# Kernel tuning notes

Measured on AMD Instinct MI355X. Metric: run time of the kernel, lower is better.

Reference implementation:

```python
import jax, jax.numpy as jnp
import numpy as np
from jax import lax

B = 65536
IMG = 28
K = 3
OUT_HW = IMG - K + 1  # 26
FLAT = OUT_HW * OUT_HW  # 676
HID = 100
NCLS = 10


def setup_inputs() -> dict:
    key = jax.random.key(0)
    ks = jax.random.split(key, 6)
    x = jax.random.normal(ks[0], (B, IMG * IMG), dtype=jnp.float32)
    conv_w = jax.random.normal(ks[1], (K, K), dtype=jnp.float32)
    # Linear params, PyTorch layout: weight [out, in], bias [out]
    w1 = jax.random.normal(ks[2], (HID, FLAT), dtype=jnp.float32) * (1.0 / np.sqrt(FLAT))
    b1 = jax.random.normal(ks[3], (HID,), dtype=jnp.float32) * 0.01
    w2 = jax.random.normal(ks[4], (NCLS, HID), dtype=jnp.float32) * (1.0 / np.sqrt(HID))
    b2 = jax.random.normal(ks[5], (NCLS,), dtype=jnp.float32) * 0.01
    return {"x": x, "conv_w": conv_w, "w1": w1, "b1": b1, "w2": w2, "b2": b2}


def reference(x, conv_w, w1, b1, w2, b2):
    # x: [B, 784] -> [B, 1, 28, 28]
    img = x.reshape(-1, 1, IMG, IMG)
    # Cross-correlation (matches the slice*weight sum in Convolve), valid padding
    kern = conv_w[None, None, :, :]  # [O=1, I=1, 3, 3]
    conv = lax.conv_general_dilated(
        img, kern, window_strides=(1, 1), padding="VALID",
        dimension_numbers=("NCHW", "OIHW", "NCHW"),
    )  # [B, 1, 26, 26]
    feat = conv.reshape(conv.shape[0], FLAT)
    h1 = jax.nn.relu(feat @ w1.T + b1)
    return h1 @ w2.T + b2  # [B, 10]
```

## Files before the change

kernel.cpp:

```cpp
#include <hip/hip_runtime.h>

#define IMG 28
#define FLATK 784
#define OHW 26
#define FLAT 676
#define HID 100
#define NCLS 10
#define KP 800
#define BM 128

typedef __attribute__((ext_vector_type(8))) short bfrag;
typedef __attribute__((ext_vector_type(4))) float f32x4;
typedef __attribute__((ext_vector_type(4))) unsigned int u32x4;

__device__ __forceinline__ unsigned short f2bf(float f) {
    unsigned u = __float_as_uint(f);
    u = (u + 0x7fffu + ((u >> 16) & 1u)) >> 16;
    return (unsigned short)u;
}

__global__ void build_weights(const float* __restrict__ conv_w,
                              const float* __restrict__ w1,
                              const float* __restrict__ w2,
                              unsigned short* __restrict__ w1b,
                              unsigned short* __restrict__ w2b) {
    int idx = blockIdx.x * blockDim.x + threadIdx.x;
    if (idx < 128 * KP) {
        int n = idx / KP, k = idx - n * KP;
        float val = 0.f;
        if (n < HID && k < FLATK) {
            int qr = k / IMG, qc = k % IMG;
            #pragma unroll
            for (int i = 0; i < 3; ++i) {
                int r = qr - i;
                if (r < 0 || r >= OHW) continue;
                #pragma unroll
                for (int j = 0; j < 3; ++j) {
                    int c = qc - j;
                    if (c < 0 || c >= OHW) continue;
                    val += conv_w[i * 3 + j] * w1[n * FLAT + r * OHW + c];
                }
            }
        }
        w1b[idx] = f2bf(val);
    } else {
        int t = idx - 128 * KP;
        if (t < 16 * 128) {
            int n = t >> 7, k = t & 127;
            float v = (n < NCLS && k < HID) ? w2[n * HID + k] : 0.f;
            w2b[t] = f2bf(v);
        }
    }
}

#define LOADA(PH, S) do {                                                      \
    int k_ = (S) * 32 + (khi << 3);                                            \
    if (k_ >= FLATK) k_ -= FLATK;     \
    pre[PH][0] = *(const f32x4*)(xr0 + k_);                                    \
    pre[PH][1] = *(const f32x4*)(xr0 + k_ + 4);                                \
    pre[PH][2] = *(const f32x4*)(xr1 + k_);                                    \
    pre[PH][3] = *(const f32x4*)(xr1 + k_ + 4);                                \
} while (0)

#define COMP(PH, S) do {                                                       \
    union { u32x4 u; bfrag b; } a0_, a1_;                                      \
    asm("v_cvt_pk_bf16_f32 %0, %1, %2" : "=v"(a0_.u.x) : "v"(pre[PH][0].x), "v"(pre[PH][0].y)); \
    asm("v_cvt_pk_bf16_f32 %0, %1, %2" : "=v"(a0_.u.y) : "v"(pre[PH][0].z), "v"(pre[PH][0].w)); \
    asm("v_cvt_pk_bf16_f32 %0, %1, %2" : "=v"(a0_.u.z) : "v"(pre[PH][1].x), "v"(pre[PH][1].y)); \
    asm("v_cvt_pk_bf16_f32 %0, %1, %2" : "=v"(a0_.u.w) : "v"(pre[PH][1].z), "v"(pre[PH][1].w)); \
    asm("v_cvt_pk_bf16_f32 %0, %1, %2" : "=v"(a1_.u.x) : "v"(pre[PH][2].x), "v"(pre[PH][2].y)); \
    asm("v_cvt_pk_bf16_f32 %0, %1, %2" : "=v"(a1_.u.y) : "v"(pre[PH][2].z), "v"(pre[PH][2].w)); \
    asm("v_cvt_pk_bf16_f32 %0, %1, %2" : "=v"(a1_.u.z) : "v"(pre[PH][3].x), "v"(pre[PH][3].y)); \
    asm("v_cvt_pk_bf16_f32 %0, %1, %2" : "=v"(a1_.u.w) : "v"(pre[PH][3].z), "v"(pre[PH][3].w)); \
    _Pragma("unroll")                                                          \
    for (int nt = 0; nt < 8; ++nt) {                                           \
        const bfrag bw = *(const bfrag*)(w1b + (size_t)((nt << 4) + r15) * KP  \
                                         + (S) * 32 + (khi << 3));             \
        acc0[nt] = __builtin_amdgcn_mfma_f32_16x16x32_bf16(a0_.b, bw, acc0[nt], 0, 0, 0); \
        acc1[nt] = __builtin_amdgcn_mfma_f32_16x16x32_bf16(a1_.b, bw, acc1[nt], 0, 0, 0); \
    }                                                                          \
} while (0)

__global__ __launch_bounds__(256) void fused_fwd(
    const float* __restrict__ x,
    const unsigned short* __restrict__ w1b,
    const float* __restrict__ b1,
    const unsigned short* __restrict__ w2b,
    const float* __restrict__ b2,
    float* __restrict__ out)
{
    __shared__ unsigned short H1[BM][136];

    const int tid  = threadIdx.x;
    const int lane = tid & 63;
    const int wv   = tid >> 6;
    const int r15  = lane & 15;
    const int khi  = lane >> 4;
    const int row0 = blockIdx.x * BM;

    const float* xr0 = x + (size_t)(row0 + (wv << 5) + r15) * FLATK;
    const float* xr1 = xr0 + 16 * FLATK;

    f32x4 acc0[8], acc1[8];
    #pragma unroll
    for (int n = 0; n < 8; ++n) {
        acc0[n] = f32x4{0.f, 0.f, 0.f, 0.f};
        acc1[n] = f32x4{0.f, 0.f, 0.f, 0.f};
    }

    f32x4 pre[3][4];

    LOADA(0, 0); LOADA(1, 1); LOADA(2, 2);

    COMP(0, 0);  LOADA(0, 3);   COMP(1, 1);  LOADA(1, 4);   COMP(2, 2);  LOADA(2, 5);
    COMP(0, 3);  LOADA(0, 6);   COMP(1, 4);  LOADA(1, 7);   COMP(2, 5);  LOADA(2, 8);
    COMP(0, 6);  LOADA(0, 9);   COMP(1, 7);  LOADA(1, 10);  COMP(2, 8);  LOADA(2, 11);
    COMP(0, 9);  LOADA(0, 12);  COMP(1, 10); LOADA(1, 13);  COMP(2, 11); LOADA(2, 14);
    COMP(0, 12); LOADA(0, 15);  COMP(1, 13); LOADA(1, 16);  COMP(2, 14); LOADA(2, 17);
    COMP(0, 15); LOADA(0, 18);  COMP(1, 16); LOADA(1, 19);  COMP(2, 17); LOADA(2, 20);
    COMP(0, 18); LOADA(0, 21);  COMP(1, 19); LOADA(1, 22);  COMP(2, 20); LOADA(2, 23);
    COMP(0, 21); LOADA(0, 24);  COMP(1, 22);                COMP(2, 23);
    COMP(0, 24);

    #pragma unroll
    for (int nt = 0; nt < 8; ++nt) {
        int col = (nt << 4) + r15;
        float bias = (col < HID) ? b1[col] : 0.f;
        int rb0 = (wv << 5) + (khi << 2);
        #pragma unroll
        for (int q = 0; q < 4; ++q) {
            float v0 = acc0[nt][q] + bias;
            float v1 = acc1[nt][q] + bias;
            H1[rb0 + q][col]      = f2bf(fmaxf(v0, 0.f));
            H1[rb0 + 16 + q][col] = f2bf(fmaxf(v1, 0.f));
        }
    }
    __syncthreads();

    f32x4 acc2[2] = {f32x4{0.f,0.f,0.f,0.f}, f32x4{0.f,0.f,0.f,0.f}};
    #pragma unroll
    for (int ks = 0; ks < 4; ++ks) {
        const bfrag bw = *(const bfrag*)(w2b + r15 * 128 + (ks << 5) + (khi << 3));
        #pragma unroll
        for (int mf = 0; mf < 2; ++mf) {
            int r = (wv << 5) + (mf << 4) + r15;
            const bfrag ah = *(const bfrag*)&H1[r][(ks << 5) + (khi << 3)];
            acc2[mf] = __builtin_amdgcn_mfma_f32_16x16x32_bf16(ah, bw, acc2[mf], 0, 0, 0);
        }
    }

    if (r15 < NCLS) {
        float bias2 = b2[r15];
        #pragma unroll
        for (int mf = 0; mf < 2; ++mf) {
            int rbase = row0 + (wv << 5) + (mf << 4) + (khi << 2);
            #pragma unroll
            for (int q = 0; q < 4; ++q)
                out[(size_t)(rbase + q) * NCLS + r15] = acc2[mf][q] + bias2;
        }
    }
}

extern "C" void kernel_launch(void* const* d_in, const int* in_sizes, int n_in,
                              void* d_out, int out_size, void* d_ws, size_t ws_size,
                              hipStream_t stream) {
    const float* x      = (const float*)d_in[0];
    const float* conv_w = (const float*)d_in[1];
    const float* w1     = (const float*)d_in[2];
    const float* b1     = (const float*)d_in[3];
    const float* w2     = (const float*)d_in[4];
    const float* b2     = (const float*)d_in[5];
    float* out = (float*)d_out;

    unsigned short* w1b = (unsigned short*)d_ws;
    unsigned short* w2b = w1b + 128 * KP;

    build_weights<<<(128 * KP + 16 * 128 + 255) / 256, 256, 0, stream>>>(conv_w, w1, w2, w1b, w2b);
    fused_fwd<<<65536 / BM, 256, 0, stream>>>(x, w1b, b1, w2b, b2, out);
}
```

Measured before the change: 59.40 us.

## Split hidden columns across two wave groups with 512-thread blocks

Doubles the block to 8 waves, with each wave computing 64 of the 128 hidden columns for 32 rows, halving the per-wave accumulator registers to raise occupancy. The second layer is redistributed so each wave handles 16 rows. The cost is that every input row is now loaded and converted by two waves, doubling global/L2 read traffic for x.

```diff
diff --git a/kernel.cpp b/kernel.cpp
--- a/kernel.cpp
+++ b/kernel.cpp
@@ -73,15 +73,15 @@
     asm("v_cvt_pk_bf16_f32 %0, %1, %2" : "=v"(a1_.u.z) : "v"(pre[PH][3].x), "v"(pre[PH][3].y)); \
     asm("v_cvt_pk_bf16_f32 %0, %1, %2" : "=v"(a1_.u.w) : "v"(pre[PH][3].z), "v"(pre[PH][3].w)); \
     _Pragma("unroll")                                                          \
-    for (int nt = 0; nt < 8; ++nt) {                                           \
-        const bfrag bw = *(const bfrag*)(w1b + (size_t)((nt << 4) + r15) * KP  \
+    for (int nt = 0; nt < 4; ++nt) {                                           \
+        const bfrag bw = *(const bfrag*)(w1b + (size_t)(ncol0 + (nt << 4) + r15) * KP \
                                          + (S) * 32 + (khi << 3));             \
         acc0[nt] = __builtin_amdgcn_mfma_f32_16x16x32_bf16(a0_.b, bw, acc0[nt], 0, 0, 0); \
         acc1[nt] = __builtin_amdgcn_mfma_f32_16x16x32_bf16(a1_.b, bw, acc1[nt], 0, 0, 0); \
     }                                                                          \
 } while (0)
 
-__global__ __launch_bounds__(256) void fused_fwd(
+__global__ __launch_bounds__(512, 4) void fused_fwd(
     const float* __restrict__ x,
     const unsigned short* __restrict__ w1b,
     const float* __restrict__ b1,
@@ -94,16 +94,19 @@
     const int tid  = threadIdx.x;
     const int lane = tid & 63;
     const int wv   = tid >> 6;
+    const int wvm  = wv & 3;
+    const int wvn  = wv >> 2;
     const int r15  = lane & 15;
     const int khi  = lane >> 4;
     const int row0 = blockIdx.x * BM;
+    const int ncol0 = wvn << 6;
 
-    const float* xr0 = x + (size_t)(row0 + (wv << 5) + r15) * FLATK;
+    const float* xr0 = x + (size_t)(row0 + (wvm << 5) + r15) * FLATK;
     const float* xr1 = xr0 + 16 * FLATK;
 
-    f32x4 acc0[8], acc1[8];
+    f32x4 acc0[4], acc1[4];
     #pragma unroll
-    for (int n = 0; n < 8; ++n) {
+    for (int n = 0; n < 4; ++n) {
         acc0[n] = f32x4{0.f, 0.f, 0.f, 0.f};
         acc1[n] = f32x4{0.f, 0.f, 0.f, 0.f};
     }
@@ -123,10 +126,10 @@
     COMP(0, 24);
 
     #pragma unroll
-    for (int nt = 0; nt < 8; ++nt) {
-        int col = (nt << 4) + r15;
+    for (int nt = 0; nt < 4; ++nt) {
+        int col = ncol0 + (nt << 4) + r15;
         float bias = (col < HID) ? b1[col] : 0.f;
-        int rb0 = (wv << 5) + (khi << 2);
+        int rb0 = (wvm << 5) + (khi << 2);
         #pragma unroll
         for (int q = 0; q < 4; ++q) {
             float v0 = acc0[nt][q] + bias;
@@ -137,27 +140,21 @@
     }
     __syncthreads();
 
-    f32x4 acc2[2] = {f32x4{0.f,0.f,0.f,0.f}, f32x4{0.f,0.f,0.f,0.f}};
+    f32x4 acc2 = f32x4{0.f, 0.f, 0.f, 0.f};
+    const int r2 = (wv << 4) + r15;
     #pragma unroll
     for (int ks = 0; ks < 4; ++ks) {
-        const bfrag bw = *(const bfrag*)(w2b + r15 * 128 + (ks << 5) + (khi << 3));
-        #pragma unroll
-        for (int mf = 0; mf < 2; ++mf) {
-            int r = (wv << 5) + (mf << 4) + r15;
-            const bfrag ah = *(const bfrag*)&H1[r][(ks << 5) + (khi << 3)];
-            acc2[mf] = __builtin_amdgcn_mfma_f32_16x16x32_bf16(ah, bw, acc2[mf], 0, 0, 0);
-        }
+        const bfrag bwv = *(const bfrag*)(w2b + r15 * 128 + (ks << 5) + (khi << 3));
+        const bfrag ah = *(const bfrag*)&H1[r2][(ks << 5) + (khi << 3)];
+        acc2 = __builtin_amdgcn_mfma_f32_16x16x32_bf16(ah, bwv, acc2, 0, 0, 0);
     }
 
     if (r15 < NCLS) {
         float bias2 = b2[r15];
+        int rbase = row0 + (wv << 4) + (khi << 2);
         #pragma unroll
-        for (int mf = 0; mf < 2; ++mf) {
-            int rbase = row0 + (wv << 5) + (mf << 4) + (khi << 2);
-            #pragma unroll
-            for (int q = 0; q < 4; ++q)
-                out[(size_t)(rbase + q) * NCLS + r15] = acc2[mf][q] + bias2;
-        }
+        for (int q = 0; q < 4; ++q)
+            out[(size_t)(rbase + q) * NCLS + r15] = acc2[q] + bias2;
     }
 }
 
@@ -176,5 +173,5 @@
     unsigned short* w2b = w1b + 128 * KP;
 
     build_weights<<<(128 * KP + 16 * 128 + 255) / 256, 256, 0, stream>>>(conv_w, w1, w2, w1b, w2b);
-    fused_fwd<<<65536 / BM, 256, 0, stream>>>(x, w1b, b1, w2b, b2, out);
+    fused_fwd<<<65536 / BM, 512, 0, stream>>>(x, w1b, b1, w2b, b2, out);
 }
```

After: 72.27 us. 1.22x slower.
